# Kernel tuning notes

Measured on AMD Instinct MI355X. Metric: run time of the kernel, lower is better.

The kernel has to match this reference:

```python
import jax, jax.numpy as jnp
import numpy as np

TEMPERATURE = 0.1
EPS = 1e-12  # matches torch F.normalize eps


def _l2_normalize(x, axis=-1):
    n = jnp.sqrt(jnp.sum(x * x, axis=axis, keepdims=True))
    return x / jnp.maximum(n, EPS)


def setup_inputs() -> dict:
    key = jax.random.key(0)
    k1, k2, k3 = jax.random.split(key, 3)
    B, K, D, M = 128, 256, 256, 4
    local_vectors = jax.random.normal(k1, (B, K, D), dtype=jnp.float32)
    prototypes = jax.random.normal(k2, (K * M, D, 1, 1), dtype=jnp.float32)
    concepts_gt = jax.random.randint(k3, (B, K), 0, 2, dtype=jnp.int32)
    return {
        "local_vectors": local_vectors,
        "prototypes": prototypes,
        "concepts_gt": concepts_gt,
        "num_prototypes_per_concept": M,
    }


def reference(local_vectors, prototypes, concepts_gt, num_prototypes_per_concept):
    B, K, D = local_vectors.shape
    M = num_prototypes_per_concept
    protos = prototypes.reshape(K * M, D)  # squeeze(-1).squeeze(-1)
    ln = _l2_normalize(local_vectors)      # (B, K, D)
    pn = _l2_normalize(protos)             # (K*M, D)

    # similarities for every (b, k) query against all prototypes in one GEMM
    sims = jnp.einsum('bkd,pd->bkp', ln, pn) / TEMPERATURE  # (B, K, K*M)

    # logsumexp over all prototypes (shared across the M positives of a concept)
    lse = jax.nn.logsumexp(sims, axis=-1)  # (B, K)

    # sum of positive similarities: prototypes k*M..(k+1)*M-1 for concept k
    # diagonal over the two K axes, summed over m
    pos_sum = jnp.einsum('bkkm->bk', sims.reshape(B, K, K, M))  # (B, K)

    mask = (concepts_gt == 1).astype(sims.dtype)  # (B, K)
    Mf = jnp.asarray(M, sims.dtype)
    total = jnp.sum(mask * (Mf * lse - pos_sum))
    count = Mf * jnp.sum(mask)
    return jnp.where(count > 0, total / jnp.maximum(count, 1.0), jnp.zeros((), sims.dtype))
```

## Files before the change

kernel.cpp:

```cpp
#include <hip/hip_runtime.h>
#include <hip/hip_bf16.h>
#include <stdint.h>

#define KC   256
#define DD   256
#define NPROT 1024
#define NQ   32768

#define OFF_TOT  0
#define OFF_CNT  8
#define OFF_PN   256
#define OFF_ACC  524544
#define ACC_STRIDE 32768

#define LN2F    0.69314718055994531f
#define C10L2E  14.426950408889634f

typedef __bf16 bf16x8 __attribute__((ext_vector_type(8)));
typedef float  f32x16 __attribute__((ext_vector_type(16)));

static __device__ __forceinline__ unsigned short f2bf(float x) {
  __hip_bfloat16 h = __float2bfloat16(x);
  return __builtin_bit_cast(unsigned short, h);
}

__global__ __launch_bounds__(256) void prep_k(const float* __restrict__ protos,
                                              unsigned char* __restrict__ ws) {
  if (blockIdx.x == 0 && threadIdx.x == 0) {
    *(float*)(ws + OFF_TOT) = 0.0f;
    *(float*)(ws + OFF_CNT) = 0.0f;
  }
  const int w = threadIdx.x >> 6, lane = threadIdx.x & 63;
  const int r = blockIdx.x * 4 + w;
  const float4 v = ((const float4*)protos)[r * 64 + lane];
  float ss = v.x*v.x + v.y*v.y + v.z*v.z + v.w*v.w;
#pragma unroll
  for (int m = 1; m < 64; m <<= 1) ss += __shfl_xor(ss, m, 64);
  const float sc = 1.0f / fmaxf(sqrtf(ss), 1e-12f);
  uint2 p;
  p.x = (unsigned)f2bf(v.x * sc) | ((unsigned)f2bf(v.y * sc) << 16);
  p.y = (unsigned)f2bf(v.z * sc) | ((unsigned)f2bf(v.w * sc) << 16);
  *(uint2*)(ws + OFF_PN + (lane >> 2) * 32768 + r * 32 + (lane & 3) * 8) = p;
}

__global__ __launch_bounds__(256) void main_k(const float* __restrict__ lv,
                                              unsigned char* __restrict__ ws) {
  __shared__ __align__(16) unsigned char Aq[64 * 512];

  const int tid  = threadIdx.x;
  const int w    = tid >> 6;
  const int lane = tid & 63;
  const int hi   = lane >> 5;
  const int l31  = lane & 31;

  const int sbid = (int)(blockIdx.x & 7) * 256 + (int)(blockIdx.x >> 3);
  const int tile = sbid >> 2;
  const int c    = sbid & 3;

  const unsigned char* pn0 = ws + OFF_PN + (c * 256 + w * 64 + l31) * 32 + hi * 16;
  const unsigned char* pn1 = pn0 + 32 * 32;

  bf16x8 pa0[2], pa1[2];
#pragma unroll
  for (int p = 0; p < 2; ++p) {
    pa0[p] = *(const bf16x8*)(pn0 + p * 32768);
    pa1[p] = *(const bf16x8*)(pn1 + p * 32768);
  }

  const int grp = tid >> 4, sub = tid & 15;
#pragma unroll
  for (int t = 0; t < 4; ++t) {
    const int r = grp * 4 + t;
    const int q = tile * 64 + r;
    float4 vv[4];
#pragma unroll
    for (int u = 0; u < 4; ++u) vv[u] = ((const float4*)lv)[q * 64 + u * 16 + sub];
    float ss = 0.0f;
#pragma unroll
    for (int u = 0; u < 4; ++u)
      ss += vv[u].x*vv[u].x + vv[u].y*vv[u].y + vv[u].z*vv[u].z + vv[u].w*vv[u].w;
#pragma unroll
    for (int m = 1; m < 16; m <<= 1) ss += __shfl_xor(ss, m, 64);
    const float sc = 1.0f / fmaxf(sqrtf(ss), 1e-12f);
    const int swz = ((r & 7) << 4) ^ (((r >> 3) & 3) << 7);
#pragma unroll
    for (int u = 0; u < 4; ++u) {
      uint2 p;
      p.x = (unsigned)f2bf(vv[u].x * sc) | ((unsigned)f2bf(vv[u].y * sc) << 16);
      p.y = (unsigned)f2bf(vv[u].z * sc) | ((unsigned)f2bf(vv[u].w * sc) << 16);
      *(uint2*)(Aq + r * 512 + ((u * 128 + sub * 8) ^ swz)) = p;
    }
  }
  __syncthreads();

  f32x16 acc[2][2];
#pragma unroll
  for (int i = 0; i < 2; ++i)
#pragma unroll
    for (int j = 0; j < 2; ++j)
#pragma unroll
      for (int t = 0; t < 16; ++t) acc[i][j][t] = 0.0f;

  const int bswz = ((l31 & 7) << 4) ^ (((l31 >> 3) & 3) << 7);

#pragma unroll
  for (int k = 0; k < 16; ++k) {
    const bf16x8 a0 = pa0[k & 1];
    const bf16x8 a1 = pa1[k & 1];
    pa0[k & 1] = *(const bf16x8*)(pn0 + ((k + 2) & 15) * 32768);
    pa1[k & 1] = *(const bf16x8*)(pn1 + ((k + 2) & 15) * 32768);
    const int bc = (k * 32 + hi * 16) ^ bswz;
    const bf16x8 b0 = *(const bf16x8*)(Aq + l31 * 512 + bc);
    const bf16x8 b1 = *(const bf16x8*)(Aq + (32 + l31) * 512 + bc);
    acc[0][0] = __builtin_amdgcn_mfma_f32_32x32x16_bf16(a0, b0, acc[0][0], 0, 0, 0);
    acc[0][1] = __builtin_amdgcn_mfma_f32_32x32x16_bf16(a0, b1, acc[0][1], 0, 0, 0);
    acc[1][0] = __builtin_amdgcn_mfma_f32_32x32x16_bf16(a1, b0, acc[1][0], 0, 0, 0);
    acc[1][1] = __builtin_amdgcn_mfma_f32_32x32x16_bf16(a1, b1, acc[1][1], 0, 0, 0);
  }

  float l_acc[2] = {0.f, 0.f}, p_acc[2] = {0.f, 0.f};
#pragma unroll
  for (int i = 0; i < 2; ++i) {
    const int r4base = c * 64 + w * 16 + i * 8 + hi;
#pragma unroll
    for (int j = 0; j < 2; ++j) {
      const int kq = (tile * 64 + j * 32 + l31) & (KC - 1);
      float l4[4] = {0.f, 0.f, 0.f, 0.f};
      float p4[4] = {0.f, 0.f, 0.f, 0.f};
#pragma unroll
      for (int g = 0; g < 4; ++g) {
        const float pm = (r4base + 2 * g == kq) ? 1.0f : 0.0f;
#pragma unroll
        for (int t = 0; t < 4; ++t) {
          const float y = acc[i][j][g * 4 + t] * C10L2E;
          l4[t] += __builtin_amdgcn_exp2f(y);
          p4[t] = fmaf(pm, y, p4[t]);
        }
      }
      l_acc[j] += (l4[0] + l4[1]) + (l4[2] + l4[3]);
      p_acc[j] += (p4[0] + p4[1]) + (p4[2] + p4[3]);
    }
  }

#pragma unroll
  for (int j = 0; j < 2; ++j) {
    l_acc[j] += __shfl_xor(l_acc[j], 32, 64);
    p_acc[j] += __shfl_xor(p_acc[j], 32, 64);
  }
  if (hi == 0) {
    float2* accb = (float2*)(ws + OFF_ACC) + (c * 4 + w) * ACC_STRIDE;
#pragma unroll
    for (int j = 0; j < 2; ++j) {
      const int q = tile * 64 + j * 32 + l31;
      float2 v2; v2.x = l_acc[j]; v2.y = p_acc[j];
      accb[q] = v2;
    }
  }
}

__global__ __launch_bounds__(256) void finish1_k(const int* __restrict__ gt,
                                                 unsigned char* __restrict__ ws) {
  __shared__ float accs[4], accn[4];
  const int i = blockIdx.x * 256 + threadIdx.x;
  float contrib = 0.0f, cnt = 0.0f;
  if (gt[i] == 1) {
    const float2* a = (const float2*)(ws + OFF_ACC);
    float L = 0.0f, P = 0.0f;
#pragma unroll
    for (int u = 0; u < 16; ++u) {
      const float2 v = a[u * ACC_STRIDE + i];
      L += v.x; P += v.y;
    }
    contrib = LN2F * (4.0f * __builtin_amdgcn_logf(L) - P);
    cnt = 1.0f;
  }
#pragma unroll
  for (int m = 1; m < 64; m <<= 1) {
    contrib += __shfl_xor(contrib, m, 64);
    cnt     += __shfl_xor(cnt, m, 64);
  }
  if ((threadIdx.x & 63) == 0) { accs[threadIdx.x >> 6] = contrib; accn[threadIdx.x >> 6] = cnt; }
  __syncthreads();
  if (threadIdx.x == 0) {
    atomicAdd((float*)(ws + OFF_TOT), (accs[0] + accs[1]) + (accs[2] + accs[3]));
    atomicAdd((float*)(ws + OFF_CNT), (accn[0] + accn[1]) + (accn[2] + accn[3]));
  }
}

__global__ __launch_bounds__(64) void finish2_k(const unsigned char* __restrict__ ws,
                                                float* __restrict__ out) {
  if (threadIdx.x == 0) {
    const float total = *(const float*)(ws + OFF_TOT);
    const float cnt   = *(const float*)(ws + OFF_CNT);
    out[0] = (cnt > 0.0f) ? total / (4.0f * cnt) : 0.0f;
  }
}

extern "C" void kernel_launch(void* const* d_in, const int* in_sizes, int n_in,
                              void* d_out, int out_size, void* d_ws, size_t ws_size,
                              hipStream_t stream) {
  const float* lv     = (const float*)d_in[0];
  const float* protos = (const float*)d_in[1];
  const int*   gt     = (const int*)d_in[2];
  (void)in_sizes; (void)n_in; (void)out_size; (void)ws_size;
  unsigned char* ws = (unsigned char*)d_ws;

  prep_k<<<256, 256, 0, stream>>>(protos, ws);
  main_k<<<2048, 256, 0, stream>>>(lv, ws);
  finish1_k<<<128, 256, 0, stream>>>(gt, ws);
  finish2_k<<<1, 64, 0, stream>>>(ws, (float*)d_out);
}
```

Baseline: 44.07 us.

## Compact masked queries and compute similarities only for positive-concept rows

Adds a compaction kernel that gathers the indices of queries with concepts_gt==1 via an atomic counter. The main GEMM kernel then processes only the compacted rows and exits early for tiles beyond the selected count. This skips roughly half of the normalization, MFMA and exp work, since masked rows never contribute. It also deepens the prototype register prefetch from 2 to 4 stages, and merges the two finish kernels into one using a last-block ticket, removing one launch. In exchange it adds an extra launch, an atomic-ordered index list that makes summation order nondeterministic, and gathered reads of local vectors.

After: 53.34 us. +21.0%, slower.

```diff
diff --git a/kernel.cpp b/kernel.cpp
--- a/kernel.cpp
+++ b/kernel.cpp
@@ -7,10 +7,12 @@
 #define NPROT 1024
 #define NQ   32768
 
-#define OFF_TOT  0
-#define OFF_CNT  8
-#define OFF_PN   256
-#define OFF_ACC  524544
+#define OFF_NSEL 0
+#define OFF_TOT  8
+#define OFF_TICK 16
+#define OFF_SEL  256
+#define OFF_PN   131328
+#define OFF_ACC  655616
 #define ACC_STRIDE 32768
 
 #define LN2F    0.69314718055994531f
@@ -27,8 +29,9 @@
 __global__ __launch_bounds__(256) void prep_k(const float* __restrict__ protos,
                                               unsigned char* __restrict__ ws) {
   if (blockIdx.x == 0 && threadIdx.x == 0) {
+    *(int*)(ws + OFF_NSEL)  = 0;
     *(float*)(ws + OFF_TOT) = 0.0f;
-    *(float*)(ws + OFF_CNT) = 0.0f;
+    *(int*)(ws + OFF_TICK)  = 0;
   }
   const int w = threadIdx.x >> 6, lane = threadIdx.x & 63;
   const int r = blockIdx.x * 4 + w;
@@ -43,6 +46,15 @@
   *(uint2*)(ws + OFF_PN + (lane >> 2) * 32768 + r * 32 + (lane & 3) * 8) = p;
 }
 
+__global__ __launch_bounds__(256) void compact_k(const int* __restrict__ gt,
+                                                 unsigned char* __restrict__ ws) {
+  const int idx = blockIdx.x * 256 + threadIdx.x;
+  if (gt[idx] == 1) {
+    int p = atomicAdd((int*)(ws + OFF_NSEL), 1);
+    ((int*)(ws + OFF_SEL))[p] = idx;
+  }
+}
+
 __global__ __launch_bounds__(256) void main_k(const float* __restrict__ lv,
                                               unsigned char* __restrict__ ws) {
   __shared__ __align__(16) unsigned char Aq[64 * 512];
@@ -53,16 +65,30 @@
   const int hi   = lane >> 5;
   const int l31  = lane & 31;
 
-  const int sbid = (int)(blockIdx.x & 7) * 256 + (int)(blockIdx.x >> 3);
+  const int sbid = (int)((blockIdx.x & 7) << 8) | (int)(blockIdx.x >> 3);
   const int tile = sbid >> 2;
   const int c    = sbid & 3;
 
+  const int n_sel = *(const int*)(ws + OFF_NSEL);
+  const int base  = tile * 64;
+  if (base >= n_sel) return;
+  const int* sel = (const int*)(ws + OFF_SEL);
+
+  int valid[2], kqr[2];
+#pragma unroll
+  for (int j = 0; j < 2; ++j) {
+    const int slot = base + j * 32 + l31;
+    valid[j] = slot < n_sel;
+    const int q = valid[j] ? sel[slot] : sel[base];
+    kqr[j] = q & (KC - 1);
+  }
+
   const unsigned char* pn0 = ws + OFF_PN + (c * 256 + w * 64 + l31) * 32 + hi * 16;
   const unsigned char* pn1 = pn0 + 32 * 32;
 
-  bf16x8 pa0[2], pa1[2];
-#pragma unroll
-  for (int p = 0; p < 2; ++p) {
+  bf16x8 pa0[4], pa1[4];
+#pragma unroll
+  for (int p = 0; p < 4; ++p) {
     pa0[p] = *(const bf16x8*)(pn0 + p * 32768);
     pa1[p] = *(const bf16x8*)(pn1 + p * 32768);
   }
@@ -70,11 +96,12 @@
   const int grp = tid >> 4, sub = tid & 15;
 #pragma unroll
   for (int t = 0; t < 4; ++t) {
-    const int r = grp * 4 + t;
-    const int q = tile * 64 + r;
+    const int r    = grp * 4 + t;
+    const int slot = base + r;
+    const int qi   = (slot < n_sel) ? sel[slot] : sel[base];
     float4 vv[4];
 #pragma unroll
-    for (int u = 0; u < 4; ++u) vv[u] = ((const float4*)lv)[q * 64 + u * 16 + sub];
+    for (int u = 0; u < 4; ++u) vv[u] = ((const float4*)lv)[qi * 64 + u * 16 + sub];
     float ss = 0.0f;
 #pragma unroll
     for (int u = 0; u < 4; ++u)
@@ -105,10 +132,10 @@
 
 #pragma unroll
   for (int k = 0; k < 16; ++k) {
-    const bf16x8 a0 = pa0[k & 1];
-    const bf16x8 a1 = pa1[k & 1];
-    pa0[k & 1] = *(const bf16x8*)(pn0 + ((k + 2) & 15) * 32768);
-    pa1[k & 1] = *(const bf16x8*)(pn1 + ((k + 2) & 15) * 32768);
+    const bf16x8 a0 = pa0[k & 3];
+    const bf16x8 a1 = pa1[k & 3];
+    pa0[k & 3] = *(const bf16x8*)(pn0 + ((k + 4) & 15) * 32768);
+    pa1[k & 3] = *(const bf16x8*)(pn1 + ((k + 4) & 15) * 32768);
     const int bc = (k * 32 + hi * 16) ^ bswz;
     const bf16x8 b0 = *(const bf16x8*)(Aq + l31 * 512 + bc);
     const bf16x8 b1 = *(const bf16x8*)(Aq + (32 + l31) * 512 + bc);
@@ -124,12 +151,11 @@
     const int r4base = c * 64 + w * 16 + i * 8 + hi;
 #pragma unroll
     for (int j = 0; j < 2; ++j) {
-      const int kq = (tile * 64 + j * 32 + l31) & (KC - 1);
       float l4[4] = {0.f, 0.f, 0.f, 0.f};
       float p4[4] = {0.f, 0.f, 0.f, 0.f};
 #pragma unroll
       for (int g = 0; g < 4; ++g) {
-        const float pm = (r4base + 2 * g == kq) ? 1.0f : 0.0f;
+        const float pm = (r4base + 2 * g == kqr[j]) ? 1.0f : 0.0f;
 #pragma unroll
         for (int t = 0; t < 4; ++t) {
           const float y = acc[i][j][g * 4 + t] * C10L2E;
@@ -151,19 +177,22 @@
     float2* accb = (float2*)(ws + OFF_ACC) + (c * 4 + w) * ACC_STRIDE;
 #pragma unroll
     for (int j = 0; j < 2; ++j) {
-      const int q = tile * 64 + j * 32 + l31;
-      float2 v2; v2.x = l_acc[j]; v2.y = p_acc[j];
-      accb[q] = v2;
-    }
-  }
-}
-
-__global__ __launch_bounds__(256) void finish1_k(const int* __restrict__ gt,
-                                                 unsigned char* __restrict__ ws) {
-  __shared__ float accs[4], accn[4];
+      if (valid[j]) {
+        const int slot = base + j * 32 + l31;
+        float2 v2; v2.x = l_acc[j]; v2.y = p_acc[j];
+        accb[slot] = v2;
+      }
+    }
+  }
+}
+
+__global__ __launch_bounds__(256) void finish_k(unsigned char* __restrict__ ws,
+                                                float* __restrict__ out) {
+  __shared__ float accs[4];
+  const int n_sel = *(const int*)(ws + OFF_NSEL);
   const int i = blockIdx.x * 256 + threadIdx.x;
-  float contrib = 0.0f, cnt = 0.0f;
-  if (gt[i] == 1) {
+  float contrib = 0.0f;
+  if (i < n_sel) {
     const float2* a = (const float2*)(ws + OFF_ACC);
     float L = 0.0f, P = 0.0f;
 #pragma unroll
@@ -172,27 +201,19 @@
       L += v.x; P += v.y;
     }
     contrib = LN2F * (4.0f * __builtin_amdgcn_logf(L) - P);
-    cnt = 1.0f;
-  }
-#pragma unroll
-  for (int m = 1; m < 64; m <<= 1) {
-    contrib += __shfl_xor(contrib, m, 64);
-    cnt     += __shfl_xor(cnt, m, 64);
-  }
-  if ((threadIdx.x & 63) == 0) { accs[threadIdx.x >> 6] = contrib; accn[threadIdx.x >> 6] = cnt; }
+  }
+#pragma unroll
+  for (int m = 1; m < 64; m <<= 1) contrib += __shfl_xor(contrib, m, 64);
+  if ((threadIdx.x & 63) == 0) accs[threadIdx.x >> 6] = contrib;
   __syncthreads();
   if (threadIdx.x == 0) {
     atomicAdd((float*)(ws + OFF_TOT), (accs[0] + accs[1]) + (accs[2] + accs[3]));
-    atomicAdd((float*)(ws + OFF_CNT), (accn[0] + accn[1]) + (accn[2] + accn[3]));
-  }
-}
-
-__global__ __launch_bounds__(64) void finish2_k(const unsigned char* __restrict__ ws,
-                                                float* __restrict__ out) {
-  if (threadIdx.x == 0) {
-    const float total = *(const float*)(ws + OFF_TOT);
-    const float cnt   = *(const float*)(ws + OFF_CNT);
-    out[0] = (cnt > 0.0f) ? total / (4.0f * cnt) : 0.0f;
+    __threadfence();
+    const int t = atomicAdd((int*)(ws + OFF_TICK), 1);
+    if (t == 127) {
+      const float total = atomicAdd((float*)(ws + OFF_TOT), 0.0f);
+      out[0] = (n_sel > 0) ? total / (4.0f * (float)n_sel) : 0.0f;
+    }
   }
 }
 
@@ -206,7 +227,7 @@
   unsigned char* ws = (unsigned char*)d_ws;
 
   prep_k<<<256, 256, 0, stream>>>(protos, ws);
+  compact_k<<<128, 256, 0, stream>>>(gt, ws);
   main_k<<<2048, 256, 0, stream>>>(lv, ws);
-  finish1_k<<<128, 256, 0, stream>>>(gt, ws);
-  finish2_k<<<1, 64, 0, stream>>>(ws, (float*)d_out);
-}
+  finish_k<<<128, 256, 0, stream>>>(ws, (float*)d_out);
+}
```
